# Performance work log

Measured on AMD Instinct MI355X. Metric: run time of the kernel, lower is better.

## Reference

```python
import jax, jax.numpy as jnp
import numpy as np

B, N, F, C, HD = 16, 2048, 1024, 256, 64  # batch, points, feat_dims, channels, head dim
EPS_BN = 1e-5

def conv1d(w, x, b=None):
    # 1x1 Conv1d: w [O,C], x [B,C,N] -> [B,O,N]
    y = jnp.einsum('oc,bcn->bon', w, x)
    return y if b is None else y + b[None, :, None]

def batchnorm(x, g, b):
    # training-mode BN over (batch, length) per channel, biased variance
    m = x.mean(axis=(0, 2), keepdims=True)
    v = x.var(axis=(0, 2), keepdims=True)
    return g[None, :, None] * (x - m) * jax.lax.rsqrt(v + EPS_BN) + b[None, :, None]

def leaky(x):
    return jnp.where(x > 0, x, 0.2 * x)

def oa_layer(x, qk_w, qk_b, v_w, v_b, t_w, t_b, bn_g, bn_b):
    # x: [B,256,N]; q and k share weights (q_conv.weight = k_conv.weight)
    q = conv1d(qk_w, x, qk_b).transpose(0, 2, 1)      # [B,N,64]
    k = conv1d(qk_w, x, qk_b)                         # [B,64,N]
    v = conv1d(v_w, x, v_b)                           # [B,256,N]
    energy = jnp.einsum('bnc,bcm->bnm', q, k)         # [B,N,N]
    att = jax.nn.softmax(energy, axis=-1)
    att = att / (1e-9 + att.sum(axis=1, keepdims=True))  # L1 renorm over columns
    x_r = jnp.einsum('bcn,bnm->bcm', v, att)          # [B,256,N]
    x_r = leaky(batchnorm(conv1d(t_w, x - x_r, t_b), bn_g, bn_b))
    return x + x_r

def setup_inputs() -> dict:
    key = jax.random.key(0)
    ks = jax.random.split(key, 20)
    s = lambda fan: 1.0 / np.sqrt(fan)
    inp = {
        'feature': jax.random.normal(ks[0], (B, 1, F), jnp.float32),
        'prior': jax.random.normal(ks[1], (B, 3, N), jnp.float32),
        'mlp_w': jax.random.normal(ks[2], (C, F + 3), jnp.float32) * s(F + 3),
        'mlp_b': jax.random.normal(ks[3], (C,), jnp.float32) * 0.01,
        'qk_w': jax.random.normal(ks[4], (4, HD, C), jnp.float32) * s(C),
        'qk_b': jax.random.normal(ks[5], (4, HD), jnp.float32) * 0.01,
        'v_w': jax.random.normal(ks[6], (4, C, C), jnp.float32) * s(C),
        'v_b': jax.random.normal(ks[7], (4, C), jnp.float32) * 0.01,
        't_w': jax.random.normal(ks[8], (4, C, C), jnp.float32) * s(C),
        't_b': jax.random.normal(ks[9], (4, C), jnp.float32) * 0.01,
        'bn_g': jnp.ones((4, C), jnp.float32),
        'bn_b': jnp.zeros((4, C), jnp.float32),
        'dc1_w': jax.random.normal(ks[10], (C, 4 * C), jnp.float32) * s(4 * C),
        'dc1_bn_g': jnp.ones((C,), jnp.float32),
        'dc1_bn_b': jnp.zeros((C,), jnp.float32),
        'dc2_w': jax.random.normal(ks[11], (3, C), jnp.float32) * s(C),
        'dc2_b': jax.random.normal(ks[12], (3,), jnp.float32) * 0.01,
        'dc2_bn_g': jnp.ones((3,), jnp.float32),
        'dc2_bn_b': jnp.zeros((3,), jnp.float32),
    }
    return inp

def reference(feature, prior, mlp_w, mlp_b, qk_w, qk_b, v_w, v_b, t_w, t_b,
              bn_g, bn_b, dc1_w, dc1_bn_g, dc1_bn_b, dc2_w, dc2_b,
              dc2_bn_g, dc2_bn_b):
    n = prior.shape[2]
    feat = jnp.broadcast_to(feature.transpose(0, 2, 1), (feature.shape[0], feature.shape[2], n))
    p = conv1d(mlp_w, jnp.concatenate([feat, prior], axis=1), mlp_b)  # [B,256,N]
    outs = []
    for i in range(4):
        p = oa_layer(p, qk_w[i], qk_b[i], v_w[i], v_b[i], t_w[i], t_b[i], bn_g[i], bn_b[i])
        outs.append(p)
    pc = jnp.concatenate(outs, axis=1)                                # [B,1024,N]
    h = leaky(batchnorm(conv1d(dc1_w, pc), dc1_bn_g, dc1_bn_b))
    points = jnp.tanh(batchnorm(conv1d(dc2_w, h, dc2_b), dc2_bn_g, dc2_bn_b))
    return points.transpose(0, 2, 1)                                  # [B,N,3]
```

## Files before the change

kernel.cpp:

```cpp
#include <hip/hip_runtime.h>
#include <hip/hip_bf16.h>

typedef __hip_bfloat16 bf16;
typedef unsigned short ushort_t;

constexpr int kB = 16;
constexpr int kN = 2048;
constexpr int kF = 1024;
constexpr int kC = 256;
constexpr int kH = 64;

using f32x4 = __attribute__((ext_vector_type(4))) float;
using bf16x8 = __attribute__((ext_vector_type(8))) short;

__device__ __forceinline__ float us2f(unsigned short u) {
  union { unsigned int i; float f; } w;
  w.i = ((unsigned int)u) << 16;
  return w.f;
}
__device__ __forceinline__ unsigned short f2bu(float f) {
  union { bf16 h; unsigned short s; } u;
  u.h = __float2bfloat16(f);
  return u.s;
}

__global__ __launch_bounds__(256) void k_fb(const float* __restrict__ feat,
                                            const float* __restrict__ mlp_w,
                                            const float* __restrict__ mlp_b,
                                            float* __restrict__ fb) {
  const int b = blockIdx.x >> 8;
  const int c = blockIdx.x & 255;
  const int t = threadIdx.x;
  const float* wr = mlp_w + (size_t)c * (kF + 3);
  const float* fr = feat + (size_t)b * kF;
  float s = 0.f;
  for (int f = t; f < kF; f += 256) s += wr[f] * fr[f];
  __shared__ float red[256];
  red[t] = s;
  __syncthreads();
  for (int k = 128; k > 0; k >>= 1) {
    if (t < k) red[t] += red[t + k];
    __syncthreads();
  }
  if (t == 0) fb[blockIdx.x] = red[0] + mlp_b[c];
}

__global__ __launch_bounds__(256) void k_p0(const float* __restrict__ prior,
                                            const float* __restrict__ mlp_w,
                                            const float* __restrict__ fb,
                                            ushort_t* __restrict__ psh,
                                            ushort_t* __restrict__ psl) {
  const size_t i = (size_t)blockIdx.x * 256 + threadIdx.x;
  const int c = (int)(i & 255);
  const int n = (int)((i >> 8) & 2047);
  const int b = (int)(i >> 19);
  const float* wr = mlp_w + (size_t)c * (kF + 3) + kF;
  const float* pr = prior + (size_t)b * 3 * kN + n;
  const float v = fb[b * kC + c] + wr[0] * pr[0] + wr[1] * pr[kN] + wr[2] * pr[2 * kN];
  const ushort_t h = f2bu(v);
  psh[i] = h;
  psl[i] = f2bu(v - us2f(h));
}

__global__ __launch_bounds__(256) void k_wsplit(const float* __restrict__ qk_w,
                                                const float* __restrict__ v_w,
                                                const float* __restrict__ t_w,
                                                const float* __restrict__ dc1_w,
                                                ushort_t* __restrict__ wfh,
                                                ushort_t* __restrict__ wfl) {
  const int idx = blockIdx.x * 256 + threadIdx.x;
  const float* src;
  int stride, OS_;
  size_t dstoff;
  int g;
  if (idx < 8192) {
    const int l = idx >> 11; g = idx & 2047;
    src = qk_w + (size_t)l * 64 * 256; stride = 256; OS_ = 4;
    dstoff = (size_t)l * 16384;
  } else if (idx < 40960) {
    const int i2 = idx - 8192; const int l = i2 >> 13; g = i2 & 8191;
    src = v_w + (size_t)l * 256 * 256; stride = 256; OS_ = 16;
    dstoff = 65536 + (size_t)l * 65536;
  } else if (idx < 73728) {
    const int i2 = idx - 40960; const int l = i2 >> 13; g = i2 & 8191;
    src = t_w + (size_t)l * 256 * 256; stride = 256; OS_ = 16;
    dstoff = 327680 + (size_t)l * 65536;
  } else {
    const int i2 = idx - 73728; const int l = i2 >> 13; g = i2 & 8191;
    src = dc1_w + (size_t)l * 256; stride = 1024; OS_ = 16;
    dstoff = 589824 + (size_t)l * 65536;
  }
  const int kk = g / (OS_ * 64);
  const int rem = g % (OS_ * 64);
  const int osub = rem >> 6;
  const int lane = rem & 63;
  const int o = osub * 16 + (lane & 15);
  const int c = kk * 32 + (lane >> 4) * 8;
  const float* sp = src + (size_t)o * stride + c;
  ushort_t h[8], l8[8];
#pragma unroll
  for (int j = 0; j < 8; ++j) {
    const float v = sp[j];
    h[j] = f2bu(v);
    l8[j] = f2bu(v - us2f(h[j]));
  }
  *(uint4*)(wfh + dstoff + (size_t)g * 8) = *(const uint4*)h;
  *(uint4*)(wfl + dstoff + (size_t)g * 8) = *(const uint4*)l8;
}

__global__ __launch_bounds__(256) void k_qv(
    const ushort_t* __restrict__ xh, const ushort_t* __restrict__ xl,
    const ushort_t* __restrict__ wqh, const ushort_t* __restrict__ wql,
    const ushort_t* __restrict__ wvh, const ushort_t* __restrict__ wvl,
    const float* __restrict__ qbias, const float* __restrict__ vbias,
    ushort_t* __restrict__ Qh, ushort_t* __restrict__ Ql,
    bf16* __restrict__ Vo) {
  const int t = threadIdx.x;
  const int b = blockIdx.y;
  const int n0 = blockIdx.x * 64;
  const int lane = t & 63, wv = t >> 6;
  const int fr = lane & 15, fq = lane >> 4;
  const ushort_t* xbh = xh + ((size_t)b * kN + n0) * kC;
  const ushort_t* xbl = xl + ((size_t)b * kN + n0) * kC;
  f32x4 accq[4];
  f32x4 accv[4][4];
#pragma unroll
  for (int ns = 0; ns < 4; ++ns) {
    accq[ns] = (f32x4){0.f, 0.f, 0.f, 0.f};
#pragma unroll
    for (int s = 0; s < 4; ++s) accv[s][ns] = (f32x4){0.f, 0.f, 0.f, 0.f};
  }
  for (int kk = 0; kk < 8; ++kk) {
    bf16x8 bh[4], bl[4];
#pragma unroll
    for (int ns = 0; ns < 4; ++ns) {
      const size_t xi = (size_t)(ns * 16 + fr) * kC + kk * 32 + fq * 8;
      bh[ns] = *(const bf16x8*)(xbh + xi);
      bl[ns] = *(const bf16x8*)(xbl + xi);
    }
    {
      const size_t wi = (((size_t)kk * 4 + wv) * 64 + lane) * 8;
      const bf16x8 ah = *(const bf16x8*)(wqh + wi);
      const bf16x8 al = *(const bf16x8*)(wql + wi);
#pragma unroll
      for (int ns = 0; ns < 4; ++ns) {
        accq[ns] = __builtin_amdgcn_mfma_f32_16x16x32_bf16(ah, bh[ns], accq[ns], 0, 0, 0);
        accq[ns] = __builtin_amdgcn_mfma_f32_16x16x32_bf16(ah, bl[ns], accq[ns], 0, 0, 0);
        accq[ns] = __builtin_amdgcn_mfma_f32_16x16x32_bf16(al, bh[ns], accq[ns], 0, 0, 0);
      }
    }
#pragma unroll
    for (int s = 0; s < 4; ++s) {
      const size_t wi = (((size_t)kk * 16 + wv * 4 + s) * 64 + lane) * 8;
      const bf16x8 ah = *(const bf16x8*)(wvh + wi);
      const bf16x8 al = *(const bf16x8*)(wvl + wi);
#pragma unroll
      for (int ns = 0; ns < 4; ++ns) {
        accv[s][ns] = __builtin_amdgcn_mfma_f32_16x16x32_bf16(ah, bh[ns], accv[s][ns], 0, 0, 0);
        accv[s][ns] = __builtin_amdgcn_mfma_f32_16x16x32_bf16(ah, bl[ns], accv[s][ns], 0, 0, 0);
        accv[s][ns] = __builtin_amdgcn_mfma_f32_16x16x32_bf16(al, bh[ns], accv[s][ns], 0, 0, 0);
      }
    }
  }
  {
    const int o0 = wv * 16 + fq * 4;
#pragma unroll
    for (int ns = 0; ns < 4; ++ns) {
      const int n = n0 + ns * 16 + fr;
      ushort_t h4[4], l4[4];
#pragma unroll
      for (int r = 0; r < 4; ++r) {
        const float v = accq[ns][r] + qbias[o0 + r];
        h4[r] = f2bu(v);
        l4[r] = f2bu(v - us2f(h4[r]));
      }
      *(ushort4*)(Qh + ((size_t)b * kN + n) * kH + o0) = *(const ushort4*)h4;
      *(ushort4*)(Ql + ((size_t)b * kN + n) * kH + o0) = *(const ushort4*)l4;
    }
  }
#pragma unroll
  for (int s = 0; s < 4; ++s) {
    const int o0 = (wv * 4 + s) * 16 + fq * 4;
#pragma unroll
    for (int ns = 0; ns < 4; ++ns) {
      const int n = n0 + ns * 16 + fr;
#pragma unroll
      for (int r = 0; r < 4; ++r)
        Vo[((size_t)b * kC + o0 + r) * kN + n] = __float2bfloat16(accv[s][ns][r] + vbias[o0 + r]);
    }
  }
}

template <int HASQV>
__global__ __launch_bounds__(256, 2) void k_fuse(
    const ushort_t* __restrict__ yh, const ushort_t* __restrict__ yl,
    ushort_t* __restrict__ ph, ushort_t* __restrict__ pl,
    const float* __restrict__ af, const float* __restrict__ cf,
    const ushort_t* __restrict__ wqh, const ushort_t* __restrict__ wql,
    const ushort_t* __restrict__ wvh, const ushort_t* __restrict__ wvl,
    const ushort_t* __restrict__ wdh, const ushort_t* __restrict__ wdl,
    const float* __restrict__ qbias, const float* __restrict__ vbias,
    ushort_t* __restrict__ Qh, ushort_t* __restrict__ Ql,
    bf16* __restrict__ Vo, float* __restrict__ hacc) {
  __shared__ __align__(16) ushort_t Sh[64][140];
  __shared__ __align__(16) ushort_t Sl[64][140];
  const int t = threadIdx.x;
  const int b = blockIdx.y;
  const int n0 = blockIdx.x * 64;
  const int lane = t & 63, wv = t >> 6;
  const int fr = lane & 15, fq = lane >> 4;
  const size_t rowbase = ((size_t)b * kN + n0) * kC;
  f32x4 accq[4];
  f32x4 accv[4][4];
  f32x4 accd[4][4];
#pragma unroll
  for (int ns = 0; ns < 4; ++ns) {
    accq[ns] = (f32x4){0.f, 0.f, 0.f, 0.f};
#pragma unroll
    for (int s = 0; s < 4; ++s) {
      accv[s][ns] = (f32x4){0.f, 0.f, 0.f, 0.f};
      accd[s][ns] = (f32x4){0.f, 0.f, 0.f, 0.f};
    }
  }
  for (int half = 0; half < 2; ++half) {
    {
      const int kkw = half * 4 + wv;
      const int cbase = kkw * 32 + fq * 8;
      const float4 a4a = *(const float4*)(af + cbase);
      const float4 a4b = *(const float4*)(af + cbase + 4);
      const float4 c4a = *(const float4*)(cf + cbase);
      const float4 c4b = *(const float4*)(cf + cbase + 4);
      const float av[8] = {a4a.x, a4a.y, a4a.z, a4a.w, a4b.x, a4b.y, a4b.z, a4b.w};
      const float cv[8] = {c4a.x, c4a.y, c4a.z, c4a.w, c4b.x, c4b.y, c4b.z, c4b.w};
      const int lcol = wv * 32 + fq * 8;
#pragma unroll
      for (int ns = 0; ns < 4; ++ns) {
        const size_t idx = rowbase + (size_t)(ns * 16 + fr) * kC + cbase;
        ushort_t yh8[8], yl8[8], p8h[8], p8l[8], nh8[8], nl8[8];
        *(uint4*)yh8 = *(const uint4*)(yh + idx);
        *(uint4*)yl8 = *(const uint4*)(yl + idx);
        *(uint4*)p8h = *(const uint4*)(ph + idx);
        *(uint4*)p8l = *(const uint4*)(pl + idx);
#pragma unroll
        for (int j = 0; j < 8; ++j) {
          const float yv = us2f(yh8[j]) + us2f(yl8[j]);
          float z = av[j] * yv + cv[j];
          z = z > 0.f ? z : 0.2f * z;
          const float pv = us2f(p8h[j]) + us2f(p8l[j]) + z;
          nh8[j] = f2bu(pv);
          nl8[j] = f2bu(pv - us2f(nh8[j]));
        }
        *(uint4*)(ph + idx) = *(const uint4*)nh8;
        *(uint4*)(pl + idx) = *(const uint4*)nl8;
        *(uint4*)&Sh[ns * 16 + fr][lcol] = *(const uint4*)nh8;
        *(uint4*)&Sl[ns * 16 + fr][lcol] = *(const uint4*)nl8;
      }
    }
    __syncthreads();
#pragma unroll
    for (int kkl = 0; kkl < 4; ++kkl) {
      const int kk = half * 4 + kkl;
      bf16x8 bh[4], bl[4];
#pragma unroll
      for (int ns = 0; ns < 4; ++ns) {
        bh[ns] = *(const bf16x8*)&Sh[ns * 16 + fr][kkl * 32 + fq * 8];
        bl[ns] = *(const bf16x8*)&Sl[ns * 16 + fr][kkl * 32 + fq * 8];
      }
      if (HASQV) {
        const size_t wi = (((size_t)kk * 4 + wv) * 64 + lane) * 8;
        const bf16x8 ah = *(const bf16x8*)(wqh + wi);
        const bf16x8 al = *(const bf16x8*)(wql + wi);
#pragma unroll
        for (int ns = 0; ns < 4; ++ns) {
          accq[ns] = __builtin_amdgcn_mfma_f32_16x16x32_bf16(ah, bh[ns], accq[ns], 0, 0, 0);
          accq[ns] = __builtin_amdgcn_mfma_f32_16x16x32_bf16(ah, bl[ns], accq[ns], 0, 0, 0);
          accq[ns] = __builtin_amdgcn_mfma_f32_16x16x32_bf16(al, bh[ns], accq[ns], 0, 0, 0);
        }
#pragma unroll
        for (int s = 0; s < 4; ++s) {
          const size_t wi2 = (((size_t)kk * 16 + wv * 4 + s) * 64 + lane) * 8;
          const bf16x8 vh = *(const bf16x8*)(wvh + wi2);
          const bf16x8 vl = *(const bf16x8*)(wvl + wi2);
#pragma unroll
          for (int ns = 0; ns < 4; ++ns) {
            accv[s][ns] = __builtin_amdgcn_mfma_f32_16x16x32_bf16(vh, bh[ns], accv[s][ns], 0, 0, 0);
            accv[s][ns] = __builtin_amdgcn_mfma_f32_16x16x32_bf16(vh, bl[ns], accv[s][ns], 0, 0, 0);
            accv[s][ns] = __builtin_amdgcn_mfma_f32_16x16x32_bf16(vl, bh[ns], accv[s][ns], 0, 0, 0);
          }
        }
      }
#pragma unroll
      for (int s = 0; s < 4; ++s) {
        const size_t wi3 = (((size_t)kk * 16 + wv * 4 + s) * 64 + lane) * 8;
        const bf16x8 dh = *(const bf16x8*)(wdh + wi3);
        const bf16x8 dl = *(const bf16x8*)(wdl + wi3);
#pragma unroll
        for (int ns = 0; ns < 4; ++ns) {
          accd[s][ns] = __builtin_amdgcn_mfma_f32_16x16x32_bf16(dh, bh[ns], accd[s][ns], 0, 0, 0);
          accd[s][ns] = __builtin_amdgcn_mfma_f32_16x16x32_bf16(dh, bl[ns], accd[s][ns], 0, 0, 0);
          accd[s][ns] = __builtin_amdgcn_mfma_f32_16x16x32_bf16(dl, bh[ns], accd[s][ns], 0, 0, 0);
        }
      }
    }
    __syncthreads();
  }
  if (HASQV) {
    const int o0 = wv * 16 + fq * 4;
#pragma unroll
    for (int ns = 0; ns < 4; ++ns) {
      const int n = n0 + ns * 16 + fr;
      ushort_t h4[4], l4[4];
#pragma unroll
      for (int r = 0; r < 4; ++r) {
        const float v = accq[ns][r] + qbias[o0 + r];
        h4[r] = f2bu(v);
        l4[r] = f2bu(v - us2f(h4[r]));
      }
      *(ushort4*)(Qh + ((size_t)b * kN + n) * kH + o0) = *(const ushort4*)h4;
      *(ushort4*)(Ql + ((size_t)b * kN + n) * kH + o0) = *(const ushort4*)l4;
    }
#pragma unroll
    for (int s = 0; s < 4; ++s) {
      const int oV = (wv * 4 + s) * 16 + fq * 4;
#pragma unroll
      for (int ns = 0; ns < 4; ++ns) {
        const int n = n0 + ns * 16 + fr;
#pragma unroll
        for (int r = 0; r < 4; ++r)
          Vo[((size_t)b * kC + oV + r) * kN + n] =
              __float2bfloat16(accv[s][ns][r] + vbias[oV + r]);
      }
    }
  }
#pragma unroll
  for (int s = 0; s < 4; ++s) {
    const int oD = (wv * 4 + s) * 16 + fq * 4;
#pragma unroll
    for (int ns = 0; ns < 4; ++ns) {
      const int n = n0 + ns * 16 + fr;
#pragma unroll
      for (int r = 0; r < 4; ++r) {
        float* pp = hacc + ((size_t)b * kC + oD + r) * kN + n;
        *pp = *pp + accd[s][ns][r];
      }
    }
  }
}

__global__ __launch_bounds__(256) void k_tconv(
    const ushort_t* __restrict__ xh, const ushort_t* __restrict__ xl,
    const ushort_t* __restrict__ wfh, const ushort_t* __restrict__ wfl,
    const float* __restrict__ bias,
    ushort_t* __restrict__ o1, ushort_t* __restrict__ o2,
    float* __restrict__ of) {
  const int t = threadIdx.x;
  const int b = blockIdx.y;
  const int n0 = blockIdx.x * 64;
  const int lane = t & 63, wv = t >> 6;
  const int fr = lane & 15, fq = lane >> 4;
  const ushort_t* xbh = xh + ((size_t)b * kN + n0) * kC;
  const ushort_t* xbl = xl + ((size_t)b * kN + n0) * kC;
  f32x4 acc[4][4];
#pragma unroll
  for (int s = 0; s < 4; ++s)
#pragma unroll
    for (int ns = 0; ns < 4; ++ns) acc[s][ns] = (f32x4){0.f, 0.f, 0.f, 0.f};
  for (int kk = 0; kk < 8; ++kk) {
    bf16x8 bh[4], bl[4];
#pragma unroll
    for (int ns = 0; ns < 4; ++ns) {
      const size_t xi = (size_t)(ns * 16 + fr) * kC + kk * 32 + fq * 8;
      bh[ns] = *(const bf16x8*)(xbh + xi);
      bl[ns] = *(const bf16x8*)(xbl + xi);
    }
#pragma unroll
    for (int s = 0; s < 4; ++s) {
      const size_t wi = (((size_t)kk * 16 + wv * 4 + s) * 64 + lane) * 8;
      const bf16x8 ah = *(const bf16x8*)(wfh + wi);
      const bf16x8 al = *(const bf16x8*)(wfl + wi);
#pragma unroll
      for (int ns = 0; ns < 4; ++ns) {
        acc[s][ns] = __builtin_amdgcn_mfma_f32_16x16x32_bf16(ah, bh[ns], acc[s][ns], 0, 0, 0);
        acc[s][ns] = __builtin_amdgcn_mfma_f32_16x16x32_bf16(ah, bl[ns], acc[s][ns], 0, 0, 0);
        acc[s][ns] = __builtin_amdgcn_mfma_f32_16x16x32_bf16(al, bh[ns], acc[s][ns], 0, 0, 0);
      }
    }
  }
  __syncthreads();
  const int blk = blockIdx.y * gridDim.x + blockIdx.x;
#pragma unroll
  for (int s = 0; s < 4; ++s) {
    const int o0 = (wv * 4 + s) * 16 + fq * 4;
    float yv[4][4];
#pragma unroll
    for (int ns = 0; ns < 4; ++ns) {
      const int n = n0 + ns * 16 + fr;
      const size_t idx = ((size_t)b * kN + n) * kC + o0;
      ushort_t h4[4], l4[4];
#pragma unroll
      for (int r = 0; r < 4; ++r) {
        const float y = acc[s][ns][r] + bias[o0 + r];
        yv[ns][r] = y;
        h4[r] = f2bu(y);
        l4[r] = f2bu(y - us2f(h4[r]));
      }
      *(ushort4*)(o1 + idx) = *(const ushort4*)h4;
      *(ushort4*)(o2 + idx) = *(const ushort4*)l4;
    }
#pragma unroll
    for (int r = 0; r < 4; ++r) {
      float s1 = yv[0][r] + yv[1][r] + yv[2][r] + yv[3][r];
      float s2 = yv[0][r] * yv[0][r] + yv[1][r] * yv[1][r] +
                 yv[2][r] * yv[2][r] + yv[3][r] * yv[3][r];
#pragma unroll
      for (int mask = 1; mask < 16; mask <<= 1) {
        s1 += __shfl_xor(s1, mask);
        s2 += __shfl_xor(s2, mask);
      }
      if (fr == 0) {
        of[(size_t)(o0 + r) * 512 + blk] = s1;
        of[131072 + (size_t)(o0 + r) * 512 + blk] = s2;
      }
    }
  }
}

__global__ __launch_bounds__(128) void k_bnred(const float* __restrict__ part,
                                               const float* __restrict__ g,
                                               const float* __restrict__ bb,
                                               float* __restrict__ af,
                                               float* __restrict__ cf) {
  const int c = blockIdx.x, t = threadIdx.x;
  const float4 v1 = *(const float4*)&part[(size_t)c * 512 + t * 4];
  const float4 v2 = *(const float4*)&part[131072 + (size_t)c * 512 + t * 4];
  float s1 = v1.x + v1.y + v1.z + v1.w;
  float s2 = v2.x + v2.y + v2.z + v2.w;
  __shared__ float r1[128], r2[128];
  r1[t] = s1;
  r2[t] = s2;
  __syncthreads();
  for (int k = 64; k > 0; k >>= 1) {
    if (t < k) {
      r1[t] += r1[t + k];
      r2[t] += r2[t + k];
    }
    __syncthreads();
  }
  if (t == 0) {
    const float im = 1.f / (float)(kB * kN);
    const float m = r1[0] * im;
    const float var = r2[0] * im - m * m;
    const float a = g[c] * rsqrtf(var + 1e-5f);
    af[c] = a;
    cf[c] = bb[c] - a * m;
  }
}

__global__ __launch_bounds__(256) void k_rowstats(const ushort_t* __restrict__ Qhi,
                                                  const ushort_t* __restrict__ Qlo,
                                                  float* __restrict__ rmx,
                                                  float* __restrict__ rsn) {
  __shared__ __align__(16) ushort_t Bh[2][64][72];
  __shared__ __align__(16) ushort_t Bl[2][64][72];
  const int b = blockIdx.y, t = threadIdx.x;
  const int r0 = blockIdx.x * 64;
  const int lane = t & 63, w = t >> 6;
  const int fr = lane & 15, fq = lane >> 4;
  const size_t qbase = (size_t)b * kN * kH;
  bf16x8 ah0, ah1, al0, al1;
  {
    const ushort_t* qh = Qhi + qbase + (size_t)(r0 + w * 16 + fr) * kH;
    const ushort_t* ql = Qlo + qbase + (size_t)(r0 + w * 16 + fr) * kH;
    ah0 = *(const bf16x8*)(qh + fq * 8);
    ah1 = *(const bf16x8*)(qh + 32 + fq * 8);
    al0 = *(const bf16x8*)(ql + fq * 8);
    al1 = *(const bf16x8*)(ql + 32 + fq * 8);
  }
  float mx[4] = {-3.0e38f, -3.0e38f, -3.0e38f, -3.0e38f};
  float sm[4] = {0.f, 0.f, 0.f, 0.f};
  const int srow = t >> 2, scol = (t & 3) * 16;
  {
    const ushort_t* qh = Qhi + qbase + (size_t)srow * kH + scol;
    const ushort_t* ql = Qlo + qbase + (size_t)srow * kH + scol;
    *(uint4*)&Bh[0][srow][scol] = *(const uint4*)qh;
    *(uint4*)&Bh[0][srow][scol + 8] = *(const uint4*)(qh + 8);
    *(uint4*)&Bl[0][srow][scol] = *(const uint4*)ql;
    *(uint4*)&Bl[0][srow][scol + 8] = *(const uint4*)(ql + 8);
  }
  __syncthreads();
  int cur = 0;
  for (int m0 = 0; m0 < kN; m0 += 64) {
    uint4 rh0, rh1, rl0, rl1;
    const bool pf = (m0 + 64 < kN);
    if (pf) {
      const ushort_t* qh = Qhi + qbase + (size_t)(m0 + 64 + srow) * kH + scol;
      const ushort_t* ql = Qlo + qbase + (size_t)(m0 + 64 + srow) * kH + scol;
      rh0 = *(const uint4*)qh;
      rh1 = *(const uint4*)(qh + 8);
      rl0 = *(const uint4*)ql;
      rl1 = *(const uint4*)(ql + 8);
    }
    float ev[4][4];
#pragma unroll
    for (int cs = 0; cs < 4; ++cs) {
      const bf16x8 bh0 = *(const bf16x8*)&Bh[cur][cs * 16 + fr][fq * 8];
      const bf16x8 bh1 = *(const bf16x8*)&Bh[cur][cs * 16 + fr][32 + fq * 8];
      const bf16x8 bl0 = *(const bf16x8*)&Bl[cur][cs * 16 + fr][fq * 8];
      const bf16x8 bl1 = *(const bf16x8*)&Bl[cur][cs * 16 + fr][32 + fq * 8];
      f32x4 e = {0.f, 0.f, 0.f, 0.f};
      e = __builtin_amdgcn_mfma_f32_16x16x32_bf16(ah0, bh0, e, 0, 0, 0);
      e = __builtin_amdgcn_mfma_f32_16x16x32_bf16(ah1, bh1, e, 0, 0, 0);
      e = __builtin_amdgcn_mfma_f32_16x16x32_bf16(ah0, bl0, e, 0, 0, 0);
      e = __builtin_amdgcn_mfma_f32_16x16x32_bf16(ah1, bl1, e, 0, 0, 0);
      e = __builtin_amdgcn_mfma_f32_16x16x32_bf16(al0, bh0, e, 0, 0, 0);
      e = __builtin_amdgcn_mfma_f32_16x16x32_bf16(al1, bh1, e, 0, 0, 0);
      ev[cs][0] = e[0]; ev[cs][1] = e[1]; ev[cs][2] = e[2]; ev[cs][3] = e[3];
    }
#pragma unroll
    for (int r = 0; r < 4; ++r) {
      const float tmax = fmaxf(fmaxf(ev[0][r], ev[1][r]), fmaxf(ev[2][r], ev[3][r]));
      const float nm = fmaxf(mx[r], tmax);
      sm[r] = sm[r] * __expf(mx[r] - nm) + __expf(ev[0][r] - nm) + __expf(ev[1][r] - nm) +
              __expf(ev[2][r] - nm) + __expf(ev[3][r] - nm);
      mx[r] = nm;
    }
    if (pf) {
      *(uint4*)&Bh[cur ^ 1][srow][scol] = rh0;
      *(uint4*)&Bh[cur ^ 1][srow][scol + 8] = rh1;
      *(uint4*)&Bl[cur ^ 1][srow][scol] = rl0;
      *(uint4*)&Bl[cur ^ 1][srow][scol + 8] = rl1;
    }
    __syncthreads();
    cur ^= 1;
  }
#pragma unroll
  for (int mask = 1; mask < 16; mask <<= 1) {
#pragma unroll
    for (int r = 0; r < 4; ++r) {
      const float om = __shfl_xor(mx[r], mask);
      const float os = __shfl_xor(sm[r], mask);
      const float nm = fmaxf(mx[r], om);
      sm[r] = sm[r] * __expf(mx[r] - nm) + os * __expf(om - nm);
      mx[r] = nm;
    }
  }
  if (fr == 0) {
#pragma unroll
    for (int r = 0; r < 4; ++r) {
      const int row = r0 + w * 16 + fq * 4 + r;
      rmx[(size_t)b * kN + row] = mx[r];
      rsn[(size_t)b * kN + row] = 1.f / sm[r];
    }
  }
}

__global__ __launch_bounds__(256) void k_colpass(const ushort_t* __restrict__ Qhi,
                                                 const ushort_t* __restrict__ Qlo,
                                                 const bf16* __restrict__ V,
                                                 const float* __restrict__ rmx,
                                                 const float* __restrict__ rsn,
                                                 const ushort_t* __restrict__ psh,
                                                 const ushort_t* __restrict__ psl,
                                                 ushort_t* __restrict__ ush,
                                                 ushort_t* __restrict__ usl) {
  constexpr int MT = 64, NT = 32;
  __shared__ __align__(16) ushort_t Anh[2][NT][72];
  __shared__ __align__(16) ushort_t Anl[2][NT][72];
  __shared__ __align__(16) ushort_t Vs[2][kC][40];
  __shared__ __align__(16) ushort_t Pl[MT][40];
  __shared__ float CsI[MT];
  const int t = threadIdx.x;
  const int b = blockIdx.y;
  const int mBase = blockIdx.x * MT;
  const size_t qbase = (size_t)b * kN * kH;
  const ushort_t* Vb_ = (const ushort_t*)V + (size_t)b * kC * kN;
  const int lane = t & 63, wv = t >> 6;
  const int fr = lane & 15, fq = lane >> 4;
  bf16x8 bmh0, bmh1, bml0, bml1;
  {
    const ushort_t* qh = Qhi + qbase + (size_t)(mBase + wv * 16 + fr) * kH;
    const ushort_t* ql = Qlo + qbase + (size_t)(mBase + wv * 16 + fr) * kH;
    bmh0 = *(const bf16x8*)(qh + fq * 8);
    bmh1 = *(const bf16x8*)(qh + 32 + fq * 8);
    bml0 = *(const bf16x8*)(ql + fq * 8);
    bml1 = *(const bf16x8*)(ql + 32 + fq * 8);
  }
  f32x4 acc[4][4];
#pragma unroll
  for (int i = 0; i < 4; ++i)
#pragma unroll
    for (int j = 0; j < 4; ++j) acc[i][j] = (f32x4){0.f, 0.f, 0.f, 0.f};
  float csloc = 0.f;
  const int arow = t >> 3, acol = (t & 7) * 8;
  const int vc = t >> 2, vq = t & 3;
  {
    *(uint4*)&Anh[0][arow][acol] = *(const uint4*)(Qhi + qbase + (size_t)arow * kH + acol);
    *(uint4*)&Anl[0][arow][acol] = *(const uint4*)(Qlo + qbase + (size_t)arow * kH + acol);
#pragma unroll
    for (int it = 0; it < 4; ++it) {
      const int c = it * 64 + vc;
      *(uint4*)&Vs[0][c][vq * 8] = *(const uint4*)(Vb_ + (size_t)c * kN + vq * 8);
    }
  }
  __syncthreads();
  int cur = 0;
  for (int n0 = 0; n0 < kN; n0 += NT) {
    uint4 rAh, rAl, rV0, rV1, rV2, rV3;
    const bool pf = (n0 + NT < kN);
    if (pf) {
      const int nn = n0 + NT;
      rAh = *(const uint4*)(Qhi + qbase + (size_t)(nn + arow) * kH + acol);
      rAl = *(const uint4*)(Qlo + qbase + (size_t)(nn + arow) * kH + acol);
      rV0 = *(const uint4*)(Vb_ + (size_t)(0 * 64 + vc) * kN + nn + vq * 8);
      rV1 = *(const uint4*)(Vb_ + (size_t)(1 * 64 + vc) * kN + nn + vq * 8);
      rV2 = *(const uint4*)(Vb_ + (size_t)(2 * 64 + vc) * kN + nn + vq * 8);
      rV3 = *(const uint4*)(Vb_ + (size_t)(3 * 64 + vc) * kN + nn + vq * 8);
    }
    const float4 rm0 = *(const float4*)&rmx[(size_t)b * kN + n0 + fq * 4];
    const float4 rm1 = *(const float4*)&rmx[(size_t)b * kN + n0 + 16 + fq * 4];
    const float4 rs0 = *(const float4*)&rsn[(size_t)b * kN + n0 + fq * 4];
    const float4 rs1 = *(const float4*)&rsn[(size_t)b * kN + n0 + 16 + fq * 4];
#pragma unroll
    for (int ns = 0; ns < 2; ++ns) {
      const bf16x8 ah0 = *(const bf16x8*)&Anh[cur][ns * 16 + fr][fq * 8];
      const bf16x8 ah1 = *(const bf16x8*)&Anh[cur][ns * 16 + fr][32 + fq * 8];
      const bf16x8 al0 = *(const bf16x8*)&Anl[cur][ns * 16 + fr][fq * 8];
      const bf16x8 al1 = *(const bf16x8*)&Anl[cur][ns * 16 + fr][32 + fq * 8];
      f32x4 e = {0.f, 0.f, 0.f, 0.f};
      e = __builtin_amdgcn_mfma_f32_16x16x32_bf16(ah0, bmh0, e, 0, 0, 0);
      e = __builtin_amdgcn_mfma_f32_16x16x32_bf16(ah1, bmh1, e, 0, 0, 0);
      e = __builtin_amdgcn_mfma_f32_16x16x32_bf16(ah0, bml0, e, 0, 0, 0);
      e = __builtin_amdgcn_mfma_f32_16x16x32_bf16(ah1, bml1, e, 0, 0, 0);
      e = __builtin_amdgcn_mfma_f32_16x16x32_bf16(al0, bmh0, e, 0, 0, 0);
      e = __builtin_amdgcn_mfma_f32_16x16x32_bf16(al1, bmh1, e, 0, 0, 0);
      const float4 rm = ns ? rm1 : rm0;
      const float4 rs = ns ? rs1 : rs0;
      ushort_t p4[4];
      {
        const float p0 = __expf(e[0] - rm.x) * rs.x;
        const float p1 = __expf(e[1] - rm.y) * rs.y;
        const float p2 = __expf(e[2] - rm.z) * rs.z;
        const float p3 = __expf(e[3] - rm.w) * rs.w;
        p4[0] = f2bu(p0); p4[1] = f2bu(p1); p4[2] = f2bu(p2); p4[3] = f2bu(p3);
        csloc += p0 + p1 + p2 + p3;
      }
      *(ushort4*)&Pl[wv * 16 + fr][ns * 16 + fq * 4] = *(const ushort4*)p4;
    }
    __syncthreads();
    bf16x8 am[4], bv[4];
#pragma unroll
    for (int ms = 0; ms < 4; ++ms)
      am[ms] = *(const bf16x8*)&Pl[ms * 16 + fr][fq * 8];
#pragma unroll
    for (int cs = 0; cs < 4; ++cs)
      bv[cs] = *(const bf16x8*)&Vs[cur][wv * 64 + cs * 16 + fr][fq * 8];
#pragma unroll
    for (int ms = 0; ms < 4; ++ms)
#pragma unroll
      for (int cs = 0; cs < 4; ++cs)
        acc[ms][cs] = __builtin_amdgcn_mfma_f32_16x16x32_bf16(am[ms], bv[cs], acc[ms][cs], 0, 0, 0);
    if (pf) {
      *(uint4*)&Anh[cur ^ 1][arow][acol] = rAh;
      *(uint4*)&Anl[cur ^ 1][arow][acol] = rAl;
      *(uint4*)&Vs[cur ^ 1][0 * 64 + vc][vq * 8] = rV0;
      *(uint4*)&Vs[cur ^ 1][1 * 64 + vc][vq * 8] = rV1;
      *(uint4*)&Vs[cur ^ 1][2 * 64 + vc][vq * 8] = rV2;
      *(uint4*)&Vs[cur ^ 1][3 * 64 + vc][vq * 8] = rV3;
    }
    __syncthreads();
    cur ^= 1;
  }
  csloc += __shfl_xor(csloc, 16);
  csloc += __shfl_xor(csloc, 32);
  if (fq == 0) CsI[wv * 16 + fr] = 1.f / (1e-9f + csloc);
  __syncthreads();
#pragma unroll
  for (int ms = 0; ms < 4; ++ms) {
#pragma unroll
    for (int r = 0; r < 4; ++r) {
      const int ml = ms * 16 + fq * 4 + r;
      const float inv = CsI[ml];
      const size_t row = ((size_t)b * kN + mBase + ml) * kC;
#pragma unroll
      for (int cs = 0; cs < 4; ++cs) {
        const int c = wv * 64 + cs * 16 + fr;
        const float xv = us2f(psh[row + c]) + us2f(psl[row + c]);
        const float u = xv - acc[ms][cs][r] * inv;
        const ushort_t h = f2bu(u);
        ush[row + c] = h;
        usl[row + c] = f2bu(u - us2f(h));
      }
    }
  }
}

__global__ __launch_bounds__(256) void k_bnstats(const float* __restrict__ y, int nch,
                                                 float* __restrict__ mean,
                                                 float* __restrict__ rsig) {
  const int c = blockIdx.x, t = threadIdx.x;
  float s = 0.f, s2 = 0.f;
  for (int b = 0; b < kB; ++b) {
    const float* p = y + ((size_t)b * nch + c) * kN;
    for (int n = t; n < kN; n += 256) {
      const float v = p[n];
      s += v;
      s2 += v * v;
    }
  }
  __shared__ float r1[256], r2[256];
  r1[t] = s;
  r2[t] = s2;
  __syncthreads();
  for (int k = 128; k > 0; k >>= 1) {
    if (t < k) {
      r1[t] += r1[t + k];
      r2[t] += r2[t + k];
    }
    __syncthreads();
  }
  if (t == 0) {
    const float im = 1.f / (float)(kB * kN);
    const float m = r1[0] * im;
    const float var = r2[0] * im - m * m;
    mean[c] = m;
    rsig[c] = rsqrtf(var + 1e-5f);
  }
}

__global__ __launch_bounds__(256) void k_dc2(const float* __restrict__ h,
                                             const float* __restrict__ mean,
                                             const float* __restrict__ rsig,
                                             const float* __restrict__ g,
                                             const float* __restrict__ bb,
                                             const float* __restrict__ w,
                                             const float* __restrict__ d2b,
                                             float* __restrict__ tpre) {
  __shared__ float wS[3][kC];
  __shared__ float aS[kC], cS[kC];
  const int t = threadIdx.x, b = blockIdx.y;
  const int n = blockIdx.x * 256 + t;
  {
    const float a = g[t] * rsig[t];
    aS[t] = a;
    cS[t] = bb[t] - a * mean[t];
    wS[0][t] = w[t];
    wS[1][t] = w[kC + t];
    wS[2][t] = w[2 * kC + t];
  }
  __syncthreads();
  float a0 = d2b[0], a1 = d2b[1], a2 = d2b[2];
  const float* hb = h + (size_t)b * kC * kN + n;
  for (int c = 0; c < kC; ++c) {
    float z = hb[(size_t)c * kN] * aS[c] + cS[c];
    z = z > 0.f ? z : 0.2f * z;
    a0 += wS[0][c] * z;
    a1 += wS[1][c] * z;
    a2 += wS[2][c] * z;
  }
  tpre[((size_t)b * 3 + 0) * kN + n] = a0;
  tpre[((size_t)b * 3 + 1) * kN + n] = a1;
  tpre[((size_t)b * 3 + 2) * kN + n] = a2;
}

__global__ __launch_bounds__(256) void k_final(const float* __restrict__ tpre,
                                               const float* __restrict__ mean,
                                               const float* __restrict__ rsig,
                                               const float* __restrict__ g,
                                               const float* __restrict__ bb,
                                               float* __restrict__ out) {
  const int i = blockIdx.x * 256 + threadIdx.x;
  const int n = i & (kN - 1), b = i >> 11;
#pragma unroll
  for (int j = 0; j < 3; ++j) {
    const float v = tpre[((size_t)b * 3 + j) * kN + n];
    const float z = g[j] * (v - mean[j]) * rsig[j] + bb[j];
    out[(size_t)i * 3 + j] = tanhf(z);
  }
}

extern "C" void kernel_launch(void* const* d_in, const int* in_sizes, int n_in,
                              void* d_out, int out_size, void* d_ws, size_t ws_size,
                              hipStream_t stream) {
  const float* feature  = (const float*)d_in[0];
  const float* prior    = (const float*)d_in[1];
  const float* mlp_w    = (const float*)d_in[2];
  const float* mlp_b    = (const float*)d_in[3];
  const float* qk_w     = (const float*)d_in[4];
  const float* qk_b     = (const float*)d_in[5];
  const float* v_w      = (const float*)d_in[6];
  const float* v_b      = (const float*)d_in[7];
  const float* t_w      = (const float*)d_in[8];
  const float* t_b      = (const float*)d_in[9];
  const float* bn_g     = (const float*)d_in[10];
  const float* bn_b     = (const float*)d_in[11];
  const float* dc1_w    = (const float*)d_in[12];
  const float* dc1_bn_g = (const float*)d_in[13];
  const float* dc1_bn_b = (const float*)d_in[14];
  const float* dc2_w    = (const float*)d_in[15];
  const float* dc2_b    = (const float*)d_in[16];
  const float* dc2_bn_g = (const float*)d_in[17];
  const float* dc2_bn_b = (const float*)d_in[18];
  float* out = (float*)d_out;

  char* base = (char*)d_ws;
  size_t off = 0;
  auto carve = [&](size_t bytes) {
    char* p = base + off;
    off += (bytes + 255) & ~(size_t)255;
    return p;
  };
  const size_t ne = (size_t)kB * kN * kC;
  ushort_t* psh  = (ushort_t*)carve(ne * 2);
  ushort_t* psl  = (ushort_t*)carve(ne * 2);
  ushort_t* ush  = (ushort_t*)carve(ne * 2);
  ushort_t* usl  = (ushort_t*)carve(ne * 2);
  float*    hacc = (float*)carve(ne * 4);
  ushort_t* Qhi  = (ushort_t*)carve((size_t)kB * kN * kH * 2);
  ushort_t* Qlo  = (ushort_t*)carve((size_t)kB * kN * kH * 2);
  bf16*     Vb   = (bf16*)carve(ne * 2);
  ushort_t* wfh  = (ushort_t*)carve((size_t)851968 * 2);
  ushort_t* wfl  = (ushort_t*)carve((size_t)851968 * 2);
  float*    part = (float*)carve((size_t)2 * 131072 * 4);
  float*    rmx  = (float*)carve((size_t)kB * kN * 4);
  float*    rsn  = (float*)carve((size_t)kB * kN * 4);
  float*    fb   = (float*)carve((size_t)kB * kC * 4);
  float*    bnm  = (float*)carve(kC * 4);
  float*    bnr  = (float*)carve(kC * 4);
  float*    tpre = (float*)carve((size_t)kB * 3 * kN * 4);

  hipMemsetAsync(hacc, 0, ne * 4, stream);
  k_wsplit<<<416, 256, 0, stream>>>(qk_w, v_w, t_w, dc1_w, wfh, wfl);
  k_fb<<<kB * kC, 256, 0, stream>>>(feature, mlp_w, mlp_b, fb);
  k_p0<<<(int)(ne / 256), 256, 0, stream>>>(prior, mlp_w, fb, psh, psl);

  const dim3 gC(kN / 64, kB);
  k_qv<<<gC, 256, 0, stream>>>(psh, psl, wfh, wfl, wfh + 65536, wfl + 65536,
                               qk_b, v_b, Qhi, Qlo, Vb);
  for (int l = 0; l < 4; ++l) {
    const size_t t_off   = 327680 + (size_t)l * 65536;
    const size_t dc1_off = 589824 + (size_t)l * 65536;
    k_rowstats<<<gC, 256, 0, stream>>>(Qhi, Qlo, rmx, rsn);
    k_colpass<<<gC, 256, 0, stream>>>(Qhi, Qlo, Vb, rmx, rsn, psh, psl, ush, usl);
    k_tconv<<<gC, 256, 0, stream>>>(ush, usl, wfh + t_off, wfl + t_off,
                                    t_b + l * kC, ush, usl, part);
    k_bnred<<<kC, 128, 0, stream>>>(part, bn_g + l * kC, bn_b + l * kC, bnm, bnr);
    if (l < 3) {
      const size_t qk_n = (size_t)(l + 1) * 16384;
      const size_t v_n  = 65536 + (size_t)(l + 1) * 65536;
      k_fuse<1><<<gC, 256, 0, stream>>>(ush, usl, psh, psl, bnm, bnr,
                                        wfh + qk_n, wfl + qk_n,
                                        wfh + v_n, wfl + v_n,
                                        wfh + dc1_off, wfl + dc1_off,
                                        qk_b + (l + 1) * kH, v_b + (l + 1) * kC,
                                        Qhi, Qlo, Vb, hacc);
    } else {
      k_fuse<0><<<gC, 256, 0, stream>>>(ush, usl, psh, psl, bnm, bnr,
                                        nullptr, nullptr, nullptr, nullptr,
                                        wfh + dc1_off, wfl + dc1_off,
                                        nullptr, nullptr,
                                        nullptr, nullptr, nullptr, hacc);
    }
  }

  k_bnstats<<<kC, 256, 0, stream>>>(hacc, kC, bnm, bnr);
  k_dc2<<<dim3(kN / 256, kB), 256, 0, stream>>>(hacc, bnm, bnr, dc1_bn_g, dc1_bn_b,
                                                dc2_w, dc2_b, tpre);
  k_bnstats<<<3, 256, 0, stream>>>(tpre, 3, bnm, bnr);
  k_final<<<(kB * kN) / 256, 256, 0, stream>>>(tpre, bnm, bnr, dc2_bn_g, dc2_bn_b, out);
}
```

Measured before the change: 1.176 ms.

## Fuse trans-conv GEMM into column attention pass and drop hacc memset

```diff
diff --git a/kernel.cpp b/kernel.cpp
--- a/kernel.cpp
+++ b/kernel.cpp
@@ -191,7 +191,7 @@
   }
 }
 
-template <int HASQV>
+template <int HASQV, int FIRST>
 __global__ __launch_bounds__(256, 2) void k_fuse(
     const ushort_t* __restrict__ yh, const ushort_t* __restrict__ yl,
     ushort_t* __restrict__ ph, ushort_t* __restrict__ pl,
@@ -341,85 +341,7 @@
 #pragma unroll
       for (int r = 0; r < 4; ++r) {
         float* pp = hacc + ((size_t)b * kC + oD + r) * kN + n;
-        *pp = *pp + accd[s][ns][r];
-      }
-    }
-  }
-}
-
-__global__ __launch_bounds__(256) void k_tconv(
-    const ushort_t* __restrict__ xh, const ushort_t* __restrict__ xl,
-    const ushort_t* __restrict__ wfh, const ushort_t* __restrict__ wfl,
-    const float* __restrict__ bias,
-    ushort_t* __restrict__ o1, ushort_t* __restrict__ o2,
-    float* __restrict__ of) {
-  const int t = threadIdx.x;
-  const int b = blockIdx.y;
-  const int n0 = blockIdx.x * 64;
-  const int lane = t & 63, wv = t >> 6;
-  const int fr = lane & 15, fq = lane >> 4;
-  const ushort_t* xbh = xh + ((size_t)b * kN + n0) * kC;
-  const ushort_t* xbl = xl + ((size_t)b * kN + n0) * kC;
-  f32x4 acc[4][4];
-#pragma unroll
-  for (int s = 0; s < 4; ++s)
-#pragma unroll
-    for (int ns = 0; ns < 4; ++ns) acc[s][ns] = (f32x4){0.f, 0.f, 0.f, 0.f};
-  for (int kk = 0; kk < 8; ++kk) {
-    bf16x8 bh[4], bl[4];
-#pragma unroll
-    for (int ns = 0; ns < 4; ++ns) {
-      const size_t xi = (size_t)(ns * 16 + fr) * kC + kk * 32 + fq * 8;
-      bh[ns] = *(const bf16x8*)(xbh + xi);
-      bl[ns] = *(const bf16x8*)(xbl + xi);
-    }
-#pragma unroll
-    for (int s = 0; s < 4; ++s) {
-      const size_t wi = (((size_t)kk * 16 + wv * 4 + s) * 64 + lane) * 8;
-      const bf16x8 ah = *(const bf16x8*)(wfh + wi);
-      const bf16x8 al = *(const bf16x8*)(wfl + wi);
-#pragma unroll
-      for (int ns = 0; ns < 4; ++ns) {
-        acc[s][ns] = __builtin_amdgcn_mfma_f32_16x16x32_bf16(ah, bh[ns], acc[s][ns], 0, 0, 0);
-        acc[s][ns] = __builtin_amdgcn_mfma_f32_16x16x32_bf16(ah, bl[ns], acc[s][ns], 0, 0, 0);
-        acc[s][ns] = __builtin_amdgcn_mfma_f32_16x16x32_bf16(al, bh[ns], acc[s][ns], 0, 0, 0);
-      }
-    }
-  }
-  __syncthreads();
-  const int blk = blockIdx.y * gridDim.x + blockIdx.x;
-#pragma unroll
-  for (int s = 0; s < 4; ++s) {
-    const int o0 = (wv * 4 + s) * 16 + fq * 4;
-    float yv[4][4];
-#pragma unroll
-    for (int ns = 0; ns < 4; ++ns) {
-      const int n = n0 + ns * 16 + fr;
-      const size_t idx = ((size_t)b * kN + n) * kC + o0;
-      ushort_t h4[4], l4[4];
-#pragma unroll
-      for (int r = 0; r < 4; ++r) {
-        const float y = acc[s][ns][r] + bias[o0 + r];
-        yv[ns][r] = y;
-        h4[r] = f2bu(y);
-        l4[r] = f2bu(y - us2f(h4[r]));
-      }
-      *(ushort4*)(o1 + idx) = *(const ushort4*)h4;
-      *(ushort4*)(o2 + idx) = *(const ushort4*)l4;
-    }
-#pragma unroll
-    for (int r = 0; r < 4; ++r) {
-      float s1 = yv[0][r] + yv[1][r] + yv[2][r] + yv[3][r];
-      float s2 = yv[0][r] * yv[0][r] + yv[1][r] * yv[1][r] +
-                 yv[2][r] * yv[2][r] + yv[3][r] * yv[3][r];
-#pragma unroll
-      for (int mask = 1; mask < 16; mask <<= 1) {
-        s1 += __shfl_xor(s1, mask);
-        s2 += __shfl_xor(s2, mask);
-      }
-      if (fr == 0) {
-        of[(size_t)(o0 + r) * 512 + blk] = s1;
-        of[131072 + (size_t)(o0 + r) * 512 + blk] = s2;
+        *pp = (FIRST ? 0.f : *pp) + accd[s][ns][r];
       }
     }
   }
@@ -554,21 +476,28 @@
   }
 }
 
-__global__ __launch_bounds__(256) void k_colpass(const ushort_t* __restrict__ Qhi,
-                                                 const ushort_t* __restrict__ Qlo,
-                                                 const bf16* __restrict__ V,
-                                                 const float* __restrict__ rmx,
-                                                 const float* __restrict__ rsn,
-                                                 const ushort_t* __restrict__ psh,
-                                                 const ushort_t* __restrict__ psl,
-                                                 ushort_t* __restrict__ ush,
-                                                 ushort_t* __restrict__ usl) {
+__global__ __launch_bounds__(256) void k_colt(const ushort_t* __restrict__ Qhi,
+                                              const ushort_t* __restrict__ Qlo,
+                                              const bf16* __restrict__ V,
+                                              const float* __restrict__ rmx,
+                                              const float* __restrict__ rsn,
+                                              const ushort_t* __restrict__ psh,
+                                              const ushort_t* __restrict__ psl,
+                                              const ushort_t* __restrict__ wth,
+                                              const ushort_t* __restrict__ wtl,
+                                              const float* __restrict__ tbias,
+                                              ushort_t* __restrict__ ush,
+                                              ushort_t* __restrict__ usl,
+                                              float* __restrict__ part) {
   constexpr int MT = 64, NT = 32;
-  __shared__ __align__(16) ushort_t Anh[2][NT][72];
-  __shared__ __align__(16) ushort_t Anl[2][NT][72];
-  __shared__ __align__(16) ushort_t Vs[2][kC][40];
-  __shared__ __align__(16) ushort_t Pl[MT][40];
-  __shared__ float CsI[MT];
+  __shared__ __align__(16) char smem[69888];
+  ushort_t (*Anh)[NT][72] = (ushort_t(*)[NT][72])(smem);
+  ushort_t (*Anl)[NT][72] = (ushort_t(*)[NT][72])(smem + 9216);
+  ushort_t (*Vs)[kC][40]  = (ushort_t(*)[kC][40])(smem + 18432);
+  ushort_t (*Pl)[40]      = (ushort_t(*)[40])(smem + 59392);
+  ushort_t (*Uh)[272]     = (ushort_t(*)[272])(smem);
+  ushort_t (*Ul)[272]     = (ushort_t(*)[272])(smem + 34816);
+  float* CsI = (float*)(smem + 69632);
   const int t = threadIdx.x;
   const int b = blockIdx.y;
   const int mBase = blockIdx.x * MT;
@@ -681,14 +610,79 @@
       const int ml = ms * 16 + fq * 4 + r;
       const float inv = CsI[ml];
       const size_t row = ((size_t)b * kN + mBase + ml) * kC;
+      const int sw = (ml & 7) << 3;
 #pragma unroll
       for (int cs = 0; cs < 4; ++cs) {
         const int c = wv * 64 + cs * 16 + fr;
         const float xv = us2f(psh[row + c]) + us2f(psl[row + c]);
         const float u = xv - acc[ms][cs][r] * inv;
         const ushort_t h = f2bu(u);
-        ush[row + c] = h;
-        usl[row + c] = f2bu(u - us2f(h));
+        Uh[ml][c ^ sw] = h;
+        Ul[ml][c ^ sw] = f2bu(u - us2f(h));
+      }
+    }
+  }
+  __syncthreads();
+  f32x4 acct[4][4];
+#pragma unroll
+  for (int s = 0; s < 4; ++s)
+#pragma unroll
+    for (int ns = 0; ns < 4; ++ns) acct[s][ns] = (f32x4){0.f, 0.f, 0.f, 0.f};
+  for (int kk = 0; kk < 8; ++kk) {
+    bf16x8 bh[4], bl[4];
+#pragma unroll
+    for (int ns = 0; ns < 4; ++ns) {
+      const int urow = ns * 16 + fr;
+      const int ucol = (kk * 32 + fq * 8) ^ ((urow & 7) << 3);
+      bh[ns] = *(const bf16x8*)&Uh[urow][ucol];
+      bl[ns] = *(const bf16x8*)&Ul[urow][ucol];
+    }
+#pragma unroll
+    for (int s = 0; s < 4; ++s) {
+      const size_t wi = (((size_t)kk * 16 + wv * 4 + s) * 64 + lane) * 8;
+      const bf16x8 ah = *(const bf16x8*)(wth + wi);
+      const bf16x8 al = *(const bf16x8*)(wtl + wi);
+#pragma unroll
+      for (int ns = 0; ns < 4; ++ns) {
+        acct[s][ns] = __builtin_amdgcn_mfma_f32_16x16x32_bf16(ah, bh[ns], acct[s][ns], 0, 0, 0);
+        acct[s][ns] = __builtin_amdgcn_mfma_f32_16x16x32_bf16(ah, bl[ns], acct[s][ns], 0, 0, 0);
+        acct[s][ns] = __builtin_amdgcn_mfma_f32_16x16x32_bf16(al, bh[ns], acct[s][ns], 0, 0, 0);
+      }
+    }
+  }
+  const int blk = blockIdx.y * gridDim.x + blockIdx.x;
+#pragma unroll
+  for (int s = 0; s < 4; ++s) {
+    const int o0 = (wv * 4 + s) * 16 + fq * 4;
+    float yv[4][4];
+#pragma unroll
+    for (int ns = 0; ns < 4; ++ns) {
+      const int n = mBase + ns * 16 + fr;
+      const size_t idx = ((size_t)b * kN + n) * kC + o0;
+      ushort_t h4[4], l4[4];
+#pragma unroll
+      for (int r = 0; r < 4; ++r) {
+        const float y = acct[s][ns][r] + tbias[o0 + r];
+        yv[ns][r] = y;
+        h4[r] = f2bu(y);
+        l4[r] = f2bu(y - us2f(h4[r]));
+      }
+      *(ushort4*)(ush + idx) = *(const ushort4*)h4;
+      *(ushort4*)(usl + idx) = *(const ushort4*)l4;
+    }
+#pragma unroll
+    for (int r = 0; r < 4; ++r) {
+      float s1 = yv[0][r] + yv[1][r] + yv[2][r] + yv[3][r];
+      float s2 = yv[0][r] * yv[0][r] + yv[1][r] * yv[1][r] +
+                 yv[2][r] * yv[2][r] + yv[3][r] * yv[3][r];
+#pragma unroll
+      for (int mask = 1; mask < 16; mask <<= 1) {
+        s1 += __shfl_xor(s1, mask);
+        s2 += __shfl_xor(s2, mask);
+      }
+      if (fr == 0) {
+        part[(size_t)(o0 + r) * 512 + blk] = s1;
+        part[131072 + (size_t)(o0 + r) * 512 + blk] = s2;
       }
     }
   }
@@ -828,7 +822,6 @@
   float*    bnr  = (float*)carve(kC * 4);
   float*    tpre = (float*)carve((size_t)kB * 3 * kN * 4);
 
-  hipMemsetAsync(hacc, 0, ne * 4, stream);
   k_wsplit<<<416, 256, 0, stream>>>(qk_w, v_w, t_w, dc1_w, wfh, wfl);
   k_fb<<<kB * kC, 256, 0, stream>>>(feature, mlp_w, mlp_b, fb);
   k_p0<<<(int)(ne / 256), 256, 0, stream>>>(prior, mlp_w, fb, psh, psl);
@@ -840,25 +833,32 @@
     const size_t t_off   = 327680 + (size_t)l * 65536;
     const size_t dc1_off = 589824 + (size_t)l * 65536;
     k_rowstats<<<gC, 256, 0, stream>>>(Qhi, Qlo, rmx, rsn);
-    k_colpass<<<gC, 256, 0, stream>>>(Qhi, Qlo, Vb, rmx, rsn, psh, psl, ush, usl);
-    k_tconv<<<gC, 256, 0, stream>>>(ush, usl, wfh + t_off, wfl + t_off,
-                                    t_b + l * kC, ush, usl, part);
+    k_colt<<<gC, 256, 0, stream>>>(Qhi, Qlo, Vb, rmx, rsn, psh, psl,
+                                   wfh + t_off, wfl + t_off, t_b + l * kC,
+                                   ush, usl, part);
     k_bnred<<<kC, 128, 0, stream>>>(part, bn_g + l * kC, bn_b + l * kC, bnm, bnr);
-    if (l < 3) {
+    if (l == 0) {
+      k_fuse<1, 1><<<gC, 256, 0, stream>>>(ush, usl, psh, psl, bnm, bnr,
+                                           wfh + 16384, wfl + 16384,
+                                           wfh + 131072, wfl + 131072,
+                                           wfh + dc1_off, wfl + dc1_off,
+                                           qk_b + kH, v_b + kC,
+                                           Qhi, Qlo, Vb, hacc);
+    } else if (l < 3) {
       const size_t qk_n = (size_t)(l + 1) * 16384;
       const size_t v_n  = 65536 + (size_t)(l + 1) * 65536;
-      k_fuse<1><<<gC, 256, 0, stream>>>(ush, usl, psh, psl, bnm, bnr,
-                                        wfh + qk_n, wfl + qk_n,
-                                        wfh + v_n, wfl + v_n,
-                                        wfh + dc1_off, wfl + dc1_off,
-                                        qk_b + (l + 1) * kH, v_b + (l + 1) * kC,
-                                        Qhi, Qlo, Vb, hacc);
+      k_fuse<1, 0><<<gC, 256, 0, stream>>>(ush, usl, psh, psl, bnm, bnr,
+                                           wfh + qk_n, wfl + qk_n,
+                                           wfh + v_n, wfl + v_n,
+                                           wfh + dc1_off, wfl + dc1_off,
+                                           qk_b + (l + 1) * kH, v_b + (l + 1) * kC,
+                                           Qhi, Qlo, Vb, hacc);
     } else {
-      k_fuse<0><<<gC, 256, 0, stream>>>(ush, usl, psh, psl, bnm, bnr,
-                                        nullptr, nullptr, nullptr, nullptr,
-                                        wfh + dc1_off, wfl + dc1_off,
-                                        nullptr, nullptr,
-                                        nullptr, nullptr, nullptr, hacc);
+      k_fuse<0, 0><<<gC, 256, 0, stream>>>(ush, usl, psh, psl, bnm, bnr,
+                                           nullptr, nullptr, nullptr, nullptr,
+                                           wfh + dc1_off, wfl + dc1_off,
+                                           nullptr, nullptr,
+                                           nullptr, nullptr, nullptr, hacc);
     }
   }
 
```

Result: faster. 1.079 ms, median of 2 (-8.2%).
